# Kernel optimization log

Measured on AMD Instinct MI355X. Metric: run time of the kernel, lower is better.

Reference implementation:

```python
import jax, jax.numpy as jnp
import numpy as np

N = 10000   # nodes
E = 160000  # edges
IN_DIM, HID, OUT_DIM = 512, 512, 256


def setup_inputs() -> dict:
    key = jax.random.key(0)
    ks = jax.random.split(key, 10)
    x = jax.random.normal(ks[0], (N, IN_DIM), dtype=jnp.float32)
    edge_index = jax.random.randint(ks[1], (2, E), 0, N, dtype=jnp.int32)
    s = 0.05
    return {
        "x": x,
        "edge_index": edge_index,
        # GIN inner MLP (iVAE-style MLP with n_layers=1 == single Linear)
        "f_W": jax.random.normal(ks[2], (IN_DIM, HID), jnp.float32) * s,
        "f_b": jnp.zeros((HID,), jnp.float32),
        # GCNConv linear
        "gcn_W": jax.random.normal(ks[3], (IN_DIM + HID, OUT_DIM), jnp.float32) * s,
        "gcn_b": jnp.zeros((OUT_DIM,), jnp.float32),
        # decode MLP: out_dim -> out_dim/2 -> 2 with relu between
        "d1_W": jax.random.normal(ks[4], (OUT_DIM, OUT_DIM // 2), jnp.float32) * s,
        "d1_b": jnp.zeros((OUT_DIM // 2,), jnp.float32),
        "d2_W": jax.random.normal(ks[5], (OUT_DIM // 2, 2), jnp.float32) * s,
        "d2_b": jnp.zeros((2,), jnp.float32),
    }


def reference(x, edge_index, f_W, f_b, gcn_W, gcn_b, d1_W, d1_b, d2_W, d2_b):
    src, dst = edge_index[0], edge_index[1]

    # ---- GINConv(f, eps=-1.0): out = f((1+eps)*x + sum_{j in N(i)} x_j)
    # eps = -1 => (1+eps) = 0, so only the neighbor sum survives.
    agg = jax.ops.segment_sum(x[src], dst, num_segments=N)      # [N, in_dim]
    h1 = agg @ f_W + f_b                                        # [N, hid]

    # (the original computes z1 = (h1-mean)/std when regularize=True, but it is
    #  overwritten before being returned -> dead code, skipped)

    # ---- GCNConv on cat(x, h1) with self-loops + symmetric normalization
    xh = jnp.concatenate((x, h1), axis=1)                       # [N, in+hid]
    h = xh @ gcn_W                                              # [N, out]

    loop = jnp.arange(N, dtype=src.dtype)
    src_f = jnp.concatenate([src, loop])                        # [E+N]
    dst_f = jnp.concatenate([dst, loop])
    deg = jax.ops.segment_sum(jnp.ones_like(dst_f, jnp.float32), dst_f,
                              num_segments=N)                   # [N]
    dis = jnp.where(deg > 0, jax.lax.rsqrt(jnp.maximum(deg, 1.0)), 0.0)
    norm = dis[src_f] * dis[dst_f]                              # [E+N]
    out = jax.ops.segment_sum(h[src_f] * norm[:, None], dst_f,
                              num_segments=N) + gcn_b           # [N, out]

    # ---- decode MLP: Linear -> relu -> Linear
    z = jax.nn.relu(out @ d1_W + d1_b)
    z1 = z @ d2_W + d2_b                                        # [N, 2]
    return z1
```

## Files before the change

### kernel.cpp

```cpp
#include <hip/hip_runtime.h>

#define N_NODES 10000
#define E_EDGES 160000
#define IN_DIM  512
#define HID_DIM 512
#define OUT_DIM 256
#define MB_T    157

typedef __attribute__((ext_vector_type(8))) short short8;
typedef __attribute__((ext_vector_type(16))) float f32x16;
typedef unsigned short u16;

__device__ __forceinline__ u16 f2bh(float f) {
  union { float f; unsigned u; } v; v.f = f;
  return (u16)((v.u + 0x7FFFu + ((v.u >> 16) & 1u)) >> 16);
}
__device__ __forceinline__ float bh2f(u16 h) {
  union { unsigned u; float f; } v; v.u = ((unsigned)h) << 16;
  return v.f;
}

__device__ __forceinline__ size_t tidx(int mb, int ktTot, int kt, int c) {
  return ((size_t)(mb * ktTot + kt) * 256 + c) * 8;
}

#define GL_LDS(gsrc, ldst)                                                      \
  __builtin_amdgcn_global_load_lds(                                             \
      (const __attribute__((address_space(1))) unsigned int*)(gsrc),            \
      (__attribute__((address_space(3))) unsigned int*)(ldst), 16, 0, 0)

__global__ void count_kernel(const int* __restrict__ dst, int* __restrict__ cnt) {
  int e = blockIdx.x * 256 + threadIdx.x;
  if (e < E_EDGES) atomicAdd(&cnt[dst[e]], 1);
}

__global__ __launch_bounds__(1024) void scan_kernel(
    int* __restrict__ cnt, int* __restrict__ row, float* __restrict__ dis) {
  __shared__ int sums[1024];
  const int CH = 10;
  int t = threadIdx.x;
  int c[CH], excl[CH];
  int s = 0;
#pragma unroll
  for (int j = 0; j < CH; ++j) {
    int idx = t * CH + j;
    c[j] = (idx < N_NODES) ? cnt[idx] : 0;
    excl[j] = s;
    s += c[j];
  }
  sums[t] = s;
  __syncthreads();
  for (int off = 1; off < 1024; off <<= 1) {
    int v = (t >= off) ? sums[t - off] : 0;
    __syncthreads();
    if (t >= off) sums[t] += v;
    __syncthreads();
  }
  int base = (t == 0) ? 0 : sums[t - 1];
#pragma unroll
  for (int j = 0; j < CH; ++j) {
    int idx = t * CH + j;
    if (idx < N_NODES) {
      int start = base + excl[j];
      row[idx] = start;
      cnt[idx] = start;
      dis[idx] = rsqrtf((float)c[j] + 1.0f);
    }
  }
  if (t == 1023) row[N_NODES] = sums[1023];
}

__global__ void place_kernel(const int* __restrict__ src, const int* __restrict__ dst,
                             int* __restrict__ cursor, int* __restrict__ col) {
  int e = blockIdx.x * 256 + threadIdx.x;
  if (e < E_EDGES) {
    int pos = atomicAdd(&cursor[dst[e]], 1);
    col[pos] = src[e];
  }
}

#define PREP_PACKX  5000
#define PREP_PACKFW 5256
#define PREP_CONVT  5320
#define PREP_TOTAL  5336

__device__ __forceinline__ void pack_row(const float* __restrict__ src,
                                         u16* __restrict__ hi, u16* __restrict__ lo,
                                         int i, int tt) {
  int k0 = tt * 4;
  float4 v = *reinterpret_cast<const float4*>(src + (size_t)i * 512 + k0);
  float a[4] = {v.x, v.y, v.z, v.w};
  ushort4 h4, l4;
  u16* hp = &h4.x; u16* lp = &l4.x;
#pragma unroll
  for (int j = 0; j < 4; ++j) {
    u16 hh = f2bh(a[j]);
    hp[j] = hh;
    lp[j] = f2bh(a[j] - bh2f(hh));
  }
  int mb = i >> 6, rl = i & 63;
  int kt = k0 >> 5, si = (k0 >> 4) & 1, kh = (k0 >> 3) & 1;
  int c = (rl >> 5) * 128 + si * 64 + kh * 32 + (rl & 31);
  size_t idx = tidx(mb, 16, kt, c) + (k0 & 7);
  *reinterpret_cast<ushort4*>(hi + idx) = h4;
  *reinterpret_cast<ushort4*>(lo + idx) = l4;
}

__global__ __launch_bounds__(256) void prep_kernel(
    const float* __restrict__ x, const float* __restrict__ f_W,
    const float* __restrict__ gcn_W, const float* __restrict__ f_b,
    u16* __restrict__ x_hi, u16* __restrict__ x_lo,
    u16* __restrict__ fWp_hi, u16* __restrict__ fWp_lo,
    u16* __restrict__ Wcomb_hi, u16* __restrict__ Wcomb_lo,
    u16* __restrict__ WbotT_hi, u16* __restrict__ WbotT_lo,
    float* __restrict__ c2) {
  __shared__ float tile[64][65];
  int b = blockIdx.x, t = threadIdx.x;

  if (b < PREP_PACKX) {
    int i = b * 2 + (t >> 7);
    pack_row(x, x_hi, x_lo, i, t & 127);
  } else if (b < PREP_PACKFW) {
    int i = (b - PREP_PACKX) * 2 + (t >> 7);
    pack_row(f_W, fWp_hi, fWp_lo, i, t & 127);
  } else if (b < PREP_CONVT) {
    int lb = b - PREP_PACKFW;
    int part = lb >> 5;
    int li = lb & 31;
    int k0g = (li >> 2) * 64;
    int n0 = (li & 3) * 64;
    const float* W = part ? (gcn_W + (size_t)IN_DIM * OUT_DIM) : gcn_W;
    u16* hi = part ? WbotT_hi : Wcomb_hi;
    u16* lo = part ? WbotT_lo : Wcomb_lo;
    int lk = t >> 4, ln = (t & 15) * 4;
#pragma unroll
    for (int p = 0; p < 4; ++p) {
      float4 v = *reinterpret_cast<const float4*>(W + (size_t)(k0g + p * 16 + lk) * 256 + n0 + ln);
      tile[p * 16 + lk][ln + 0] = v.x;
      tile[p * 16 + lk][ln + 1] = v.y;
      tile[p * 16 + lk][ln + 2] = v.z;
      tile[p * 16 + lk][ln + 3] = v.w;
    }
    __syncthreads();
    int on = t >> 2;
    int ok = (t & 3) * 16;
    int colg = n0 + on;
    int nb = colg >> 6, rl = colg & 63;
#pragma unroll
    for (int q = 0; q < 4; ++q) {
      int kg = k0g + ok + q * 4;
      ushort4 h4, l4;
      u16* hq = &h4.x; u16* lq = &l4.x;
#pragma unroll
      for (int j = 0; j < 4; ++j) {
        float v = tile[ok + q * 4 + j][on];
        u16 hh = f2bh(v);
        hq[j] = hh;
        lq[j] = f2bh(v - bh2f(hh));
      }
      int kt = kg >> 5, si = (kg >> 4) & 1, kh = (kg >> 3) & 1;
      int c = (rl >> 5) * 128 + si * 64 + kh * 32 + (rl & 31);
      size_t idx = tidx(nb, 16, kt, c) + (kg & 7);
      *reinterpret_cast<ushort4*>(hi + idx) = h4;
      *reinterpret_cast<ushort4*>(lo + idx) = l4;
    }
  } else {
    int cb = b - PREP_CONVT;
    float s = 0.f;
    int kb = cb * 32;
#pragma unroll 8
    for (int k = kb; k < kb + 32; ++k)
      s += f_b[k] * gcn_W[(size_t)(IN_DIM + k) * OUT_DIM + t];
    atomicAdd(&c2[t], s);
  }
}

template <bool BIAS, bool OUT_TILED>
__global__ __launch_bounds__(256) void mfma_gemm4(
    const u16* __restrict__ Ah0, const u16* __restrict__ Al0,
    const u16* __restrict__ Ah1, const u16* __restrict__ Al1, int kSplit,
    const u16* __restrict__ Bh, const u16* __restrict__ Bl,
    const float* __restrict__ bias, float* __restrict__ C,
    u16* __restrict__ Ch, u16* __restrict__ Cl, int M, int K, int N,
    int mbOff) {
  __shared__ short8 S[2][1024];

  int t = threadIdx.x, w = t >> 6, l = t & 63;
  int wr = w >> 1, wc = w & 1;
  int mb = blockIdx.y, nb = blockIdx.x;
  int brow = mb * 64, bcol = nb * 64;
  int cid = w * 64 + l;

  f32x16 acc0, acc1;
#pragma unroll
  for (int r = 0; r < 16; ++r) { acc0[r] = 0.f; acc1[r] = 0.f; }

  int nt = K / 32;
  int ktTotB = K >> 5;
  int ktTot0 = kSplit >> 5;
  int ktTot1 = (K - kSplit) >> 5;

#define STAGE(BUF, K0)                                                         \
  {                                                                            \
    const u16 *Ah, *Al; size_t abase;                                          \
    if ((K0) < kSplit) {                                                       \
      Ah = Ah0; Al = Al0; abase = tidx(mb, ktTot0, (K0) >> 5, cid);            \
    } else {                                                                   \
      Ah = Ah1; Al = Al1; abase = tidx(mb, ktTot1, ((K0) - kSplit) >> 5, cid); \
    }                                                                          \
    size_t bbase = tidx(nb, ktTotB, (K0) >> 5, cid);                           \
    short8* base = &S[BUF][0] + w * 64;                                        \
    GL_LDS(Ah + abase, base);                                                  \
    GL_LDS(Al + abase, base + 256);                                            \
    GL_LDS(Bh + bbase, base + 512);                                            \
    GL_LDS(Bl + bbase, base + 768);                                            \
  }

  STAGE(0, 0)
  for (int ti = 0; ti < nt; ++ti) {
    int b = ti & 1;
    __syncthreads();
    if (ti + 1 < nt) STAGE(b ^ 1, (ti + 1) * 32)
    {
      short8 ah = S[b][wr * 128 + l];
      short8 al = S[b][256 + wr * 128 + l];
      short8 bh = S[b][512 + wc * 128 + l];
      short8 bl = S[b][768 + wc * 128 + l];
      acc0 = __builtin_amdgcn_mfma_f32_32x32x16_bf16(ah, bh, acc0, 0, 0, 0);
      acc0 = __builtin_amdgcn_mfma_f32_32x32x16_bf16(al, bh, acc0, 0, 0, 0);
      acc0 = __builtin_amdgcn_mfma_f32_32x32x16_bf16(ah, bl, acc0, 0, 0, 0);
    }
    {
      short8 ah = S[b][wr * 128 + 64 + l];
      short8 al = S[b][256 + wr * 128 + 64 + l];
      short8 bh = S[b][512 + wc * 128 + 64 + l];
      short8 bl = S[b][768 + wc * 128 + 64 + l];
      acc1 = __builtin_amdgcn_mfma_f32_32x32x16_bf16(ah, bh, acc1, 0, 0, 0);
      acc1 = __builtin_amdgcn_mfma_f32_32x32x16_bf16(al, bh, acc1, 0, 0, 0);
      acc1 = __builtin_amdgcn_mfma_f32_32x32x16_bf16(ah, bl, acc1, 0, 0, 0);
    }
  }
#undef STAGE

  f32x16 acc = acc0 + acc1;

  int r0l = wr * 32 + 4 * (l >> 5);
  int c0l = wc * 32 + (l & 31);

  if (OUT_TILED) {
    __syncthreads();
    u16* Hhi = (u16*)&S[0][0];
    u16* Hlo = Hhi + 4096;
    float badd = BIAS ? bias[bcol + c0l] : 0.f;
#pragma unroll
    for (int r = 0; r < 16; ++r) {
      int rl = r0l + (r & 3) + 8 * (r >> 2);
      float v = acc[r] + badd;
      u16 hh = f2bh(v);
      Hhi[rl * 64 + c0l] = hh;
      Hlo[rl * 64 + c0l] = f2bh(v - bh2f(hh));
    }
    __syncthreads();
    int ktTot = N >> 5;
#pragma unroll
    for (int pl = 0; pl < 2; ++pl) {
      const u16* Hs = pl ? Hlo : Hhi;
      u16* dA = pl ? Cl : Ch;
#pragma unroll
      for (int j = 0; j < 2; ++j) {
        int ci = t + j * 256;
        int ktl = ci >> 8;
        int c = ci & 255;
        int r = ((c >> 7) & 1) * 32 + (c & 31);
        int kloc = ktl * 32 + ((c >> 6) & 1) * 16 + ((c >> 5) & 1) * 8;
        short8 v = *reinterpret_cast<const short8*>(Hs + r * 64 + kloc);
        size_t db = tidx(mb + mbOff, ktTot, (bcol >> 5) + ktl, c);
        *reinterpret_cast<short8*>(dA + db) = v;
      }
    }
  } else {
    int colg = bcol + c0l;
    float badd = BIAS ? bias[colg] : 0.f;
#pragma unroll
    for (int r = 0; r < 16; ++r) {
      int rowg = brow + r0l + (r & 3) + 8 * (r >> 2);
      if (rowg < M) C[(size_t)rowg * N + colg] = acc[r] + badd;
    }
  }
}

template <int NB>
__global__ __launch_bounds__(256) void zgemm_kernel(
    const u16* __restrict__ Ah, const u16* __restrict__ Al,
    const u16* __restrict__ Bh, const u16* __restrict__ Bl,
    float* __restrict__ z1, u16* __restrict__ z2b, int M, int K) {
  constexpr int BCH = NB * 256;
  __shared__ short8 S[2][512 + 2 * BCH];

  int bid = blockIdx.x;
  int X = bid & 7, sslot = bid >> 3;
  int mb = X + 8 * (sslot >> 2);
  int nbB = sslot & 3;
  if (mb >= MB_T) return;

  int t = threadIdx.x, w = t >> 6, l = t & 63;
  int wr = w >> 1, wc = w & 1;
  int cid = t;
  int ktTot = K >> 5;

  f32x16 acc[NB][2];
#pragma unroll
  for (int n = 0; n < NB; ++n)
#pragma unroll
    for (int si = 0; si < 2; ++si)
#pragma unroll
      for (int r = 0; r < 16; ++r) acc[n][si][r] = 0.f;

  int nt = K / 32;

#define ZSTAGE(BUF, K0)                                                        \
  {                                                                            \
    size_t ab = tidx(mb, ktTot, (K0) >> 5, cid);                               \
    short8* base = &S[BUF][0] + w * 64;                                        \
    GL_LDS(Ah + ab, base);                                                     \
    GL_LDS(Al + ab, base + 256);                                               \
    _Pragma("unroll") for (int j = 0; j < NB; ++j) {                           \
      size_t bb = tidx(nbB * NB + j, ktTot, (K0) >> 5, cid);                   \
      GL_LDS(Bh + bb, base + 512 + j * 256);                                   \
      GL_LDS(Bl + bb, base + 512 + BCH + j * 256);                             \
    }                                                                          \
  }

  ZSTAGE(0, 0)
  for (int ti = 0; ti < nt; ++ti) {
    int b = ti & 1;
    __syncthreads();
    if (ti + 1 < nt) ZSTAGE(b ^ 1, (ti + 1) * 32)
#pragma unroll
    for (int si = 0; si < 2; ++si) {
      short8 ah = S[b][wr * 128 + si * 64 + l];
      short8 al = S[b][256 + wr * 128 + si * 64 + l];
#pragma unroll
      for (int n2 = 0; n2 < NB; ++n2) {
        short8 bh = S[b][512 + wc * 256 + n2 * 128 + si * 64 + l];
        short8 bl = S[b][512 + BCH + wc * 256 + n2 * 128 + si * 64 + l];
        acc[n2][si] = __builtin_amdgcn_mfma_f32_32x32x16_bf16(ah, bh, acc[n2][si], 0, 0, 0);
        acc[n2][si] = __builtin_amdgcn_mfma_f32_32x32x16_bf16(al, bh, acc[n2][si], 0, 0, 0);
        acc[n2][si] = __builtin_amdgcn_mfma_f32_32x32x16_bf16(ah, bl, acc[n2][si], 0, 0, 0);
      }
    }
  }
#undef ZSTAGE

  int r0 = mb * 64 + wr * 32 + 4 * (l >> 5);
#pragma unroll
  for (int n2 = 0; n2 < NB; ++n2) {
    f32x16 a = acc[n2][0] + acc[n2][1];
    int colg = nbB * (NB * 64) + wc * 64 + n2 * 32 + (l & 31);
#pragma unroll
    for (int r = 0; r < 16; ++r) {
      int rowg = r0 + (r & 3) + 8 * (r >> 2);
      if (rowg < M) {
        float v = a[r];
        if (colg < 256) z1[(size_t)rowg * 256 + colg] = v;
        else            z2b[(size_t)rowg * 256 + colg - 256] = f2bh(v);
      }
    }
  }
}

__global__ __launch_bounds__(64) void h_build_kernel(
    const float* __restrict__ z1, const u16* __restrict__ z2b,
    const int* __restrict__ row, const int* __restrict__ col,
    const float* __restrict__ c2, float* __restrict__ h,
    u16* __restrict__ h_bf) {
  int i = blockIdx.x, t = threadIdx.x;
  int half = t >> 5, sl = t & 31;
  int beg = row[i], end = row[i + 1];

  float a0[8] = {}, a1[8] = {}, a2[8] = {}, a3[8] = {};
  int e = beg + half;
  for (; e + 6 < end; e += 8) {
    int s0 = col[e], s1 = col[e + 2], s2 = col[e + 4], s3 = col[e + 6];
    short8 v0 = *reinterpret_cast<const short8*>(z2b + (size_t)s0 * 256 + sl * 8);
    short8 v1 = *reinterpret_cast<const short8*>(z2b + (size_t)s1 * 256 + sl * 8);
    short8 v2 = *reinterpret_cast<const short8*>(z2b + (size_t)s2 * 256 + sl * 8);
    short8 v3 = *reinterpret_cast<const short8*>(z2b + (size_t)s3 * 256 + sl * 8);
#pragma unroll
    for (int j = 0; j < 8; ++j) {
      a0[j] += bh2f((u16)v0[j]);
      a1[j] += bh2f((u16)v1[j]);
      a2[j] += bh2f((u16)v2[j]);
      a3[j] += bh2f((u16)v3[j]);
    }
  }
  for (; e < end; e += 2) {
    int s = col[e];
    short8 v = *reinterpret_cast<const short8*>(z2b + (size_t)s * 256 + sl * 8);
#pragma unroll
    for (int j = 0; j < 8; ++j) a0[j] += bh2f((u16)v[j]);
  }
  float acc[8];
#pragma unroll
  for (int j = 0; j < 8; ++j) {
    acc[j] = a0[j] + a1[j] + a2[j] + a3[j];
    acc[j] += __shfl_xor(acc[j], 32);
  }
  float4 z1a = *reinterpret_cast<const float4*>(z1 + (size_t)i * 256 + sl * 8);
  float4 z1b = *reinterpret_cast<const float4*>(z1 + (size_t)i * 256 + sl * 8 + 4);
  float4 ca = *reinterpret_cast<const float4*>(c2 + sl * 8);
  float4 cb = *reinterpret_cast<const float4*>(c2 + sl * 8 + 4);
  float hv[8] = {z1a.x + ca.x + acc[0], z1a.y + ca.y + acc[1],
                 z1a.z + ca.z + acc[2], z1a.w + ca.w + acc[3],
                 z1b.x + cb.x + acc[4], z1b.y + cb.y + acc[5],
                 z1b.z + cb.z + acc[6], z1b.w + cb.w + acc[7]};
  if (half == 0) {
    float4 o0{hv[0], hv[1], hv[2], hv[3]};
    float4 o1{hv[4], hv[5], hv[6], hv[7]};
    *reinterpret_cast<float4*>(h + (size_t)i * 256 + sl * 8) = o0;
    *reinterpret_cast<float4*>(h + (size_t)i * 256 + sl * 8 + 4) = o1;
    short8 hb;
#pragma unroll
    for (int j = 0; j < 8; ++j) hb[j] = (short)f2bh(hv[j]);
    *reinterpret_cast<short8*>(h_bf + (size_t)i * 256 + sl * 8) = hb;
  }
}

__global__ __launch_bounds__(64) void gcn_gather_kernel(
    const float* __restrict__ h, const u16* __restrict__ h_bf,
    const int* __restrict__ row, const int* __restrict__ col,
    const float* __restrict__ dis, const float* __restrict__ gcn_b,
    float* __restrict__ outg) {
  int i = blockIdx.x, t = threadIdx.x;
  int half = t >> 5, sl = t & 31;
  int beg = row[i], end = row[i + 1];
  float di = dis[i];

  float a0[8] = {}, a1[8] = {}, a2[8] = {}, a3[8] = {};
  int e = beg + half;
  for (; e + 6 < end; e += 8) {
    int s0 = col[e], s1 = col[e + 2], s2 = col[e + 4], s3 = col[e + 6];
    float w0 = dis[s0], w1 = dis[s1], w2 = dis[s2], w3 = dis[s3];
    short8 v0 = *reinterpret_cast<const short8*>(h_bf + (size_t)s0 * 256 + sl * 8);
    short8 v1 = *reinterpret_cast<const short8*>(h_bf + (size_t)s1 * 256 + sl * 8);
    short8 v2 = *reinterpret_cast<const short8*>(h_bf + (size_t)s2 * 256 + sl * 8);
    short8 v3 = *reinterpret_cast<const short8*>(h_bf + (size_t)s3 * 256 + sl * 8);
#pragma unroll
    for (int j = 0; j < 8; ++j) {
      a0[j] += w0 * bh2f((u16)v0[j]);
      a1[j] += w1 * bh2f((u16)v1[j]);
      a2[j] += w2 * bh2f((u16)v2[j]);
      a3[j] += w3 * bh2f((u16)v3[j]);
    }
  }
  for (; e < end; e += 2) {
    int s = col[e];
    float wv = dis[s];
    short8 v = *reinterpret_cast<const short8*>(h_bf + (size_t)s * 256 + sl * 8);
#pragma unroll
    for (int j = 0; j < 8; ++j) a0[j] += wv * bh2f((u16)v[j]);
  }
  float acc[8];
#pragma unroll
  for (int j = 0; j < 8; ++j) {
    acc[j] = a0[j] + a1[j] + a2[j] + a3[j];
    acc[j] += __shfl_xor(acc[j], 32);
  }
  if (half == 0) {
    float4 ha = *reinterpret_cast<const float4*>(h + (size_t)i * 256 + sl * 8);
    float4 hb = *reinterpret_cast<const float4*>(h + (size_t)i * 256 + sl * 8 + 4);
    float4 ba = *reinterpret_cast<const float4*>(gcn_b + sl * 8);
    float4 bb = *reinterpret_cast<const float4*>(gcn_b + sl * 8 + 4);
    float self = di * di;
    float4 o0{di * acc[0] + self * ha.x + ba.x, di * acc[1] + self * ha.y + ba.y,
              di * acc[2] + self * ha.z + ba.z, di * acc[3] + self * ha.w + ba.w};
    float4 o1{di * acc[4] + self * hb.x + bb.x, di * acc[5] + self * hb.y + bb.y,
              di * acc[6] + self * hb.z + bb.z, di * acc[7] + self * hb.w + bb.w};
    *reinterpret_cast<float4*>(outg + (size_t)i * 256 + sl * 8) = o0;
    *reinterpret_cast<float4*>(outg + (size_t)i * 256 + sl * 8 + 4) = o1;
  }
}

#define DEC_NODES 8
__global__ __launch_bounds__(128) void decode_kernel(
    const float* __restrict__ outg, const float* __restrict__ d1_W,
    const float* __restrict__ d1_b, const float* __restrict__ d2_W,
    const float* __restrict__ d2_b, float* __restrict__ z1) {
  __shared__ float rows[DEC_NODES][OUT_DIM];
  __shared__ float s0[128], s1[128];
  int t = threadIdx.x;
  int n0 = blockIdx.x * DEC_NODES;
#pragma unroll
  for (int j = 0; j < 4; ++j) {
    int idx = j * 512 + t * 4;
    *reinterpret_cast<float4*>(&rows[0][idx]) =
        *reinterpret_cast<const float4*>(outg + (size_t)n0 * OUT_DIM + idx);
  }
  __syncthreads();
  float acc[DEC_NODES];
  float b1 = d1_b[t];
#pragma unroll
  for (int n = 0; n < DEC_NODES; ++n) acc[n] = b1;
#pragma unroll 4
  for (int k = 0; k < OUT_DIM; ++k) {
    float wv = d1_W[k * 128 + t];
#pragma unroll
    for (int n = 0; n < DEC_NODES; ++n) acc[n] += rows[n][k] * wv;
  }
  float w0 = d2_W[t * 2 + 0], w1 = d2_W[t * 2 + 1];
  for (int n = 0; n < DEC_NODES; ++n) {
    float a = fmaxf(acc[n], 0.f);
    s0[t] = a * w0;
    s1[t] = a * w1;
    __syncthreads();
    for (int off = 64; off > 0; off >>= 1) {
      if (t < off) {
        s0[t] += s0[t + off];
        s1[t] += s1[t + off];
      }
      __syncthreads();
    }
    if (t == 0) {
      z1[(size_t)(n0 + n) * 2 + 0] = s0[0] + d2_b[0];
      z1[(size_t)(n0 + n) * 2 + 1] = s1[0] + d2_b[1];
    }
    __syncthreads();
  }
}

extern "C" void kernel_launch(void* const* d_in, const int* in_sizes, int n_in,
                              void* d_out, int out_size, void* d_ws, size_t ws_size,
                              hipStream_t stream) {
  const float* x     = (const float*)d_in[0];
  const int*   edge  = (const int*)d_in[1];
  const float* f_W   = (const float*)d_in[2];
  const float* f_b   = (const float*)d_in[3];
  const float* gcn_W = (const float*)d_in[4];
  const float* gcn_b = (const float*)d_in[5];
  const float* d1_W  = (const float*)d_in[6];
  const float* d1_b  = (const float*)d_in[7];
  const float* d2_W  = (const float*)d_in[8];
  const float* d2_b  = (const float*)d_in[9];
  float* out = (float*)d_out;
  char*  wsb = (char*)d_ws;

  const int* src = edge;
  const int* dst = edge + E_EDGES;

  const size_t TS   = (size_t)MB_T * 16 * 256 * 8 * sizeof(u16);
  const size_t WTLE = (size_t)16 * 256 * 8 * sizeof(u16);

  size_t o = 0;
  u16*   x_hi = (u16*)(wsb + o); o += TS;
  u16*   x_lo = (u16*)(wsb + o); o += TS;
  float* z1   = (float*)(wsb + o); o += (size_t)N_NODES * 256 * 4;
  u16*   z2b  = (u16*)(wsb + o);   o += (size_t)N_NODES * 256 * 2;
  float* h    = (float*)(wsb + o); o += (size_t)N_NODES * 256 * 4;
  u16*   h_bf = (u16*)(wsb + o);   o += (size_t)N_NODES * 256 * 2;
  float* dis7 = (float*)(wsb + o); o += (size_t)N_NODES * 4;
  int*   icnt7 = (int*)(wsb + o);  o += (size_t)N_NODES * 4;
  float* c2   = (float*)(wsb + o); o += OUT_DIM * 4;
  int*   irow7 = (int*)(wsb + o);  o += (size_t)(N_NODES + 1) * 4 + 12;
  int*   icol7 = (int*)(wsb + o);  o += (size_t)E_EDGES * 4;
  u16*   Wcomb_hi = (u16*)(wsb + o); o += 8 * WTLE;
  u16*   Wcomb_lo = (u16*)(wsb + o); o += 8 * WTLE;
  u16*   WbotT_hi = (u16*)(wsb + o); o += 4 * WTLE;
  u16*   WbotT_lo = (u16*)(wsb + o); o += 4 * WTLE;
  u16*   fWp_hi   = (u16*)(wsb + o); o += 8 * WTLE;
  u16*   fWp_lo   = (u16*)(wsb + o); o += 8 * WTLE;
  float* outg = (float*)(wsb + 0);
  const size_t v7_needed = o;

  if (ws_size >= v7_needed) {
    hipMemsetAsync(icnt7, 0, (size_t)N_NODES * sizeof(int) + OUT_DIM * sizeof(float), stream);
    count_kernel<<<(E_EDGES + 255) / 256, 256, 0, stream>>>(dst, icnt7);
    scan_kernel<<<1, 1024, 0, stream>>>(icnt7, irow7, dis7);
    place_kernel<<<(E_EDGES + 255) / 256, 256, 0, stream>>>(src, dst, icnt7, icol7);

    prep_kernel<<<PREP_TOTAL, 256, 0, stream>>>(
        x, f_W, gcn_W, f_b, x_hi, x_lo, fWp_hi, fWp_lo,
        Wcomb_hi, Wcomb_lo, WbotT_hi, WbotT_lo, c2);

    mfma_gemm4<false, true><<<dim3(512 / 64, 256 / 64), 256, 0, stream>>>(
        WbotT_hi, WbotT_lo, WbotT_hi, WbotT_lo, HID_DIM,
        fWp_hi, fWp_lo, nullptr, nullptr, Wcomb_hi, Wcomb_lo,
        256, HID_DIM, 512, 4);

    zgemm_kernel<2><<<640, 256, 0, stream>>>(
        x_hi, x_lo, Wcomb_hi, Wcomb_lo, z1, z2b, N_NODES, IN_DIM);

    h_build_kernel<<<N_NODES, 64, 0, stream>>>(z1, z2b, irow7, icol7, c2, h, h_bf);

    gcn_gather_kernel<<<N_NODES, 64, 0, stream>>>(h, h_bf, irow7, icol7, dis7, gcn_b, outg);
    decode_kernel<<<N_NODES / DEC_NODES, 128, 0, stream>>>(outg, d1_W, d1_b, d2_W, d2_b, out);
  }
}
```

Before: 150.2 us.

## Fuse graph-CSR build stages into prep and weight-GEMM kernels to cut launches

```diff
diff --git a/kernel.cpp b/kernel.cpp
--- a/kernel.cpp
+++ b/kernel.cpp
@@ -23,22 +23,21 @@
 __device__ __forceinline__ size_t tidx(int mb, int ktTot, int kt, int c) {
   return ((size_t)(mb * ktTot + kt) * 256 + c) * 8;
 }
+__device__ __forceinline__ short8 g16(const u16* p) {
+  return *reinterpret_cast<const short8*>(p);
+}
 
 #define GL_LDS(gsrc, ldst)                                                      \
   __builtin_amdgcn_global_load_lds(                                             \
       (const __attribute__((address_space(1))) unsigned int*)(gsrc),            \
       (__attribute__((address_space(3))) unsigned int*)(ldst), 16, 0, 0)
 
-__global__ void count_kernel(const int* __restrict__ dst, int* __restrict__ cnt) {
-  int e = blockIdx.x * 256 + threadIdx.x;
-  if (e < E_EDGES) atomicAdd(&cnt[dst[e]], 1);
-}
-
 __global__ __launch_bounds__(1024) void scan_kernel(
     int* __restrict__ cnt, int* __restrict__ row, float* __restrict__ dis) {
-  __shared__ int sums[1024];
+  __shared__ int wsum[16];
   const int CH = 10;
   int t = threadIdx.x;
+  int lane = t & 63, wid = t >> 6;
   int c[CH], excl[CH];
   int s = 0;
 #pragma unroll
@@ -48,15 +47,26 @@
     excl[j] = s;
     s += c[j];
   }
-  sums[t] = s;
+  int incl = s;
+#pragma unroll
+  for (int off = 1; off < 64; off <<= 1) {
+    int v = __shfl_up(incl, off);
+    if (lane >= off) incl += v;
+  }
+  if (lane == 63) wsum[wid] = incl;
   __syncthreads();
-  for (int off = 1; off < 1024; off <<= 1) {
-    int v = (t >= off) ? sums[t - off] : 0;
-    __syncthreads();
-    if (t >= off) sums[t] += v;
-    __syncthreads();
-  }
-  int base = (t == 0) ? 0 : sums[t - 1];
+  if (t < 16) {
+    int v = wsum[t];
+#pragma unroll
+    for (int off = 1; off < 16; off <<= 1) {
+      int u = __shfl_up(v, off);
+      if (t >= off) v += u;
+    }
+    wsum[t] = v;
+  }
+  __syncthreads();
+  int waveBase = (wid == 0) ? 0 : wsum[wid - 1];
+  int base = waveBase + incl - s;
 #pragma unroll
   for (int j = 0; j < CH; ++j) {
     int idx = t * CH + j;
@@ -67,22 +77,14 @@
       dis[idx] = rsqrtf((float)c[j] + 1.0f);
     }
   }
-  if (t == 1023) row[N_NODES] = sums[1023];
-}
-
-__global__ void place_kernel(const int* __restrict__ src, const int* __restrict__ dst,
-                             int* __restrict__ cursor, int* __restrict__ col) {
-  int e = blockIdx.x * 256 + threadIdx.x;
-  if (e < E_EDGES) {
-    int pos = atomicAdd(&cursor[dst[e]], 1);
-    col[pos] = src[e];
-  }
+  if (t == 1023) row[N_NODES] = wsum[15];
 }
 
 #define PREP_PACKX  5000
 #define PREP_PACKFW 5256
 #define PREP_CONVT  5320
-#define PREP_TOTAL  5336
+#define PREP_C2END  5336
+#define PREP_TOTAL  5961
 
 __device__ __forceinline__ void pack_row(const float* __restrict__ src,
                                          u16* __restrict__ hi, u16* __restrict__ lo,
@@ -109,6 +111,7 @@
 __global__ __launch_bounds__(256) void prep_kernel(
     const float* __restrict__ x, const float* __restrict__ f_W,
     const float* __restrict__ gcn_W, const float* __restrict__ f_b,
+    const int* __restrict__ dst, int* __restrict__ icnt,
     u16* __restrict__ x_hi, u16* __restrict__ x_lo,
     u16* __restrict__ fWp_hi, u16* __restrict__ fWp_lo,
     u16* __restrict__ Wcomb_hi, u16* __restrict__ Wcomb_lo,
@@ -164,7 +167,7 @@
       *reinterpret_cast<ushort4*>(hi + idx) = h4;
       *reinterpret_cast<ushort4*>(lo + idx) = l4;
     }
-  } else {
+  } else if (b < PREP_C2END) {
     int cb = b - PREP_CONVT;
     float s = 0.f;
     int kb = cb * 32;
@@ -172,119 +175,108 @@
     for (int k = kb; k < kb + 32; ++k)
       s += f_b[k] * gcn_W[(size_t)(IN_DIM + k) * OUT_DIM + t];
     atomicAdd(&c2[t], s);
-  }
-}
-
-template <bool BIAS, bool OUT_TILED>
-__global__ __launch_bounds__(256) void mfma_gemm4(
-    const u16* __restrict__ Ah0, const u16* __restrict__ Al0,
-    const u16* __restrict__ Ah1, const u16* __restrict__ Al1, int kSplit,
-    const u16* __restrict__ Bh, const u16* __restrict__ Bl,
-    const float* __restrict__ bias, float* __restrict__ C,
-    u16* __restrict__ Ch, u16* __restrict__ Cl, int M, int K, int N,
-    int mbOff) {
-  __shared__ short8 S[2][1024];
-
-  int t = threadIdx.x, w = t >> 6, l = t & 63;
+  } else {
+    int e = (b - PREP_C2END) * 256 + t;
+    if (e < E_EDGES) atomicAdd(&icnt[dst[e]], 1);
+  }
+}
+
+#define PW_PLACE 625
+#define PW_TOTAL 657
+
+__global__ __launch_bounds__(256) void pw_kernel(
+    const int* __restrict__ src, const int* __restrict__ dst,
+    int* __restrict__ cursor, int* __restrict__ col,
+    const u16* __restrict__ WbotT_hi, const u16* __restrict__ WbotT_lo,
+    const u16* __restrict__ fWp_hi, const u16* __restrict__ fWp_lo,
+    u16* __restrict__ Wcomb_hi, u16* __restrict__ Wcomb_lo) {
+  __shared__ u16 H[8192];
+  int b = blockIdx.x, t = threadIdx.x;
+
+  if (b < PW_PLACE) {
+    int e = b * 256 + t;
+    if (e < E_EDGES) {
+      int pos = atomicAdd(&cursor[dst[e]], 1);
+      col[pos] = src[e];
+    }
+    return;
+  }
+
+  int lb = b - PW_PLACE;
+  int nb = lb & 7;
+  int mbw = lb >> 3;
+  int w = t >> 6, l = t & 63;
   int wr = w >> 1, wc = w & 1;
-  int mb = blockIdx.y, nb = blockIdx.x;
-  int brow = mb * 64, bcol = nb * 64;
-  int cid = w * 64 + l;
+  int cA = wr * 128 + l;
+  int cB = wc * 128 + l;
 
   f32x16 acc0, acc1;
 #pragma unroll
   for (int r = 0; r < 16; ++r) { acc0[r] = 0.f; acc1[r] = 0.f; }
 
-  int nt = K / 32;
-  int ktTotB = K >> 5;
-  int ktTot0 = kSplit >> 5;
-  int ktTot1 = (K - kSplit) >> 5;
-
-#define STAGE(BUF, K0)                                                         \
+#define W2LOAD(KT, AH0, AL0, BH0, BL0, AH1, AL1, BH1, BL1)                     \
   {                                                                            \
-    const u16 *Ah, *Al; size_t abase;                                          \
-    if ((K0) < kSplit) {                                                       \
-      Ah = Ah0; Al = Al0; abase = tidx(mb, ktTot0, (K0) >> 5, cid);            \
-    } else {                                                                   \
-      Ah = Ah1; Al = Al1; abase = tidx(mb, ktTot1, ((K0) - kSplit) >> 5, cid); \
-    }                                                                          \
-    size_t bbase = tidx(nb, ktTotB, (K0) >> 5, cid);                           \
-    short8* base = &S[BUF][0] + w * 64;                                        \
-    GL_LDS(Ah + abase, base);                                                  \
-    GL_LDS(Al + abase, base + 256);                                            \
-    GL_LDS(Bh + bbase, base + 512);                                            \
-    GL_LDS(Bl + bbase, base + 768);                                            \
-  }
-
-  STAGE(0, 0)
-  for (int ti = 0; ti < nt; ++ti) {
-    int b = ti & 1;
-    __syncthreads();
-    if (ti + 1 < nt) STAGE(b ^ 1, (ti + 1) * 32)
-    {
-      short8 ah = S[b][wr * 128 + l];
-      short8 al = S[b][256 + wr * 128 + l];
-      short8 bh = S[b][512 + wc * 128 + l];
-      short8 bl = S[b][768 + wc * 128 + l];
-      acc0 = __builtin_amdgcn_mfma_f32_32x32x16_bf16(ah, bh, acc0, 0, 0, 0);
-      acc0 = __builtin_amdgcn_mfma_f32_32x32x16_bf16(al, bh, acc0, 0, 0, 0);
-      acc0 = __builtin_amdgcn_mfma_f32_32x32x16_bf16(ah, bl, acc0, 0, 0, 0);
-    }
-    {
-      short8 ah = S[b][wr * 128 + 64 + l];
-      short8 al = S[b][256 + wr * 128 + 64 + l];
-      short8 bh = S[b][512 + wc * 128 + 64 + l];
-      short8 bl = S[b][768 + wc * 128 + 64 + l];
-      acc1 = __builtin_amdgcn_mfma_f32_32x32x16_bf16(ah, bh, acc1, 0, 0, 0);
-      acc1 = __builtin_amdgcn_mfma_f32_32x32x16_bf16(al, bh, acc1, 0, 0, 0);
-      acc1 = __builtin_amdgcn_mfma_f32_32x32x16_bf16(ah, bl, acc1, 0, 0, 0);
-    }
-  }
-#undef STAGE
+    size_t a0 = tidx(mbw, 16, (KT), cA);                                       \
+    size_t a1 = tidx(mbw, 16, (KT), cA + 64);                                  \
+    size_t b0 = tidx(nb, 16, (KT), cB);                                        \
+    size_t b1 = tidx(nb, 16, (KT), cB + 64);                                   \
+    AH0 = g16(WbotT_hi + a0); AL0 = g16(WbotT_lo + a0);                        \
+    BH0 = g16(fWp_hi + b0);   BL0 = g16(fWp_lo + b0);                          \
+    AH1 = g16(WbotT_hi + a1); AL1 = g16(WbotT_lo + a1);                        \
+    BH1 = g16(fWp_hi + b1);   BL1 = g16(fWp_lo + b1);                          \
+  }
+#define W2MMA(AH0, AL0, BH0, BL0, AH1, AL1, BH1, BL1)                          \
+  {                                                                            \
+    acc0 = __builtin_amdgcn_mfma_f32_32x32x16_bf16(AH0, BH0, acc0, 0, 0, 0);   \
+    acc0 = __builtin_amdgcn_mfma_f32_32x32x16_bf16(AL0, BH0, acc0, 0, 0, 0);   \
+    acc0 = __builtin_amdgcn_mfma_f32_32x32x16_bf16(AH0, BL0, acc0, 0, 0, 0);   \
+    acc1 = __builtin_amdgcn_mfma_f32_32x32x16_bf16(AH1, BH1, acc1, 0, 0, 0);   \
+    acc1 = __builtin_amdgcn_mfma_f32_32x32x16_bf16(AL1, BH1, acc1, 0, 0, 0);   \
+    acc1 = __builtin_amdgcn_mfma_f32_32x32x16_bf16(AH1, BL1, acc1, 0, 0, 0);   \
+  }
+
+  short8 xah0, xal0, xbh0, xbl0, xah1, xal1, xbh1, xbl1;
+  short8 yah0, yal0, ybh0, ybl0, yah1, yal1, ybh1, ybl1;
+  W2LOAD(0, xah0, xal0, xbh0, xbl0, xah1, xal1, xbh1, xbl1)
+#pragma unroll
+  for (int kt = 0; kt < 16; kt += 2) {
+    W2LOAD(kt + 1, yah0, yal0, ybh0, ybl0, yah1, yal1, ybh1, ybl1)
+    W2MMA(xah0, xal0, xbh0, xbl0, xah1, xal1, xbh1, xbl1)
+    if (kt + 2 < 16)
+      W2LOAD(kt + 2, xah0, xal0, xbh0, xbl0, xah1, xal1, xbh1, xbl1)
+    W2MMA(yah0, yal0, ybh0, ybl0, yah1, yal1, ybh1, ybl1)
+  }
+#undef W2LOAD
+#undef W2MMA
 
   f32x16 acc = acc0 + acc1;
-
+  u16* Hhi = H;
+  u16* Hlo = H + 4096;
   int r0l = wr * 32 + 4 * (l >> 5);
   int c0l = wc * 32 + (l & 31);
-
-  if (OUT_TILED) {
-    __syncthreads();
-    u16* Hhi = (u16*)&S[0][0];
-    u16* Hlo = Hhi + 4096;
-    float badd = BIAS ? bias[bcol + c0l] : 0.f;
-#pragma unroll
-    for (int r = 0; r < 16; ++r) {
-      int rl = r0l + (r & 3) + 8 * (r >> 2);
-      float v = acc[r] + badd;
-      u16 hh = f2bh(v);
-      Hhi[rl * 64 + c0l] = hh;
-      Hlo[rl * 64 + c0l] = f2bh(v - bh2f(hh));
-    }
-    __syncthreads();
-    int ktTot = N >> 5;
-#pragma unroll
-    for (int pl = 0; pl < 2; ++pl) {
-      const u16* Hs = pl ? Hlo : Hhi;
-      u16* dA = pl ? Cl : Ch;
-#pragma unroll
-      for (int j = 0; j < 2; ++j) {
-        int ci = t + j * 256;
-        int ktl = ci >> 8;
-        int c = ci & 255;
-        int r = ((c >> 7) & 1) * 32 + (c & 31);
-        int kloc = ktl * 32 + ((c >> 6) & 1) * 16 + ((c >> 5) & 1) * 8;
-        short8 v = *reinterpret_cast<const short8*>(Hs + r * 64 + kloc);
-        size_t db = tidx(mb + mbOff, ktTot, (bcol >> 5) + ktl, c);
-        *reinterpret_cast<short8*>(dA + db) = v;
-      }
-    }
-  } else {
-    int colg = bcol + c0l;
-    float badd = BIAS ? bias[colg] : 0.f;
-#pragma unroll
-    for (int r = 0; r < 16; ++r) {
-      int rowg = brow + r0l + (r & 3) + 8 * (r >> 2);
-      if (rowg < M) C[(size_t)rowg * N + colg] = acc[r] + badd;
+#pragma unroll
+  for (int r = 0; r < 16; ++r) {
+    int rl = r0l + (r & 3) + 8 * (r >> 2);
+    float v = acc[r];
+    u16 hh = f2bh(v);
+    Hhi[rl * 64 + c0l] = hh;
+    Hlo[rl * 64 + c0l] = f2bh(v - bh2f(hh));
+  }
+  __syncthreads();
+#pragma unroll
+  for (int pl = 0; pl < 2; ++pl) {
+    const u16* Hs = pl ? Hlo : Hhi;
+    u16* dA = pl ? Wcomb_lo : Wcomb_hi;
+#pragma unroll
+    for (int j = 0; j < 2; ++j) {
+      int ci = t + j * 256;
+      int ktl = ci >> 8;
+      int c = ci & 255;
+      int r = ((c >> 7) & 1) * 32 + (c & 31);
+      int kloc = ktl * 32 + ((c >> 6) & 1) * 16 + ((c >> 5) & 1) * 8;
+      short8 v = *reinterpret_cast<const short8*>(Hs + r * 64 + kloc);
+      size_t db = tidx(mbw + 4, 16, nb * 2 + ktl, c);
+      *reinterpret_cast<short8*>(dA + db) = v;
     }
   }
 }
@@ -369,12 +361,13 @@
   }
 }
 
-__global__ __launch_bounds__(64) void h_build_kernel(
+__global__ __launch_bounds__(128) void h_build_kernel(
     const float* __restrict__ z1, const u16* __restrict__ z2b,
     const int* __restrict__ row, const int* __restrict__ col,
     const float* __restrict__ c2, float* __restrict__ h,
     u16* __restrict__ h_bf) {
-  int i = blockIdx.x, t = threadIdx.x;
+  int i = blockIdx.x * 2 + (threadIdx.x >> 6);
+  int t = threadIdx.x & 63;
   int half = t >> 5, sl = t & 31;
   int beg = row[i], end = row[i + 1];
 
@@ -426,12 +419,13 @@
   }
 }
 
-__global__ __launch_bounds__(64) void gcn_gather_kernel(
+__global__ __launch_bounds__(128) void gcn_gather_kernel(
     const float* __restrict__ h, const u16* __restrict__ h_bf,
     const int* __restrict__ row, const int* __restrict__ col,
     const float* __restrict__ dis, const float* __restrict__ gcn_b,
     float* __restrict__ outg) {
-  int i = blockIdx.x, t = threadIdx.x;
+  int i = blockIdx.x * 2 + (threadIdx.x >> 6);
+  int t = threadIdx.x & 63;
   int half = t >> 5, sl = t & 31;
   int beg = row[i], end = row[i + 1];
   float di = dis[i];
@@ -557,11 +551,11 @@
   u16*   z2b  = (u16*)(wsb + o);   o += (size_t)N_NODES * 256 * 2;
   float* h    = (float*)(wsb + o); o += (size_t)N_NODES * 256 * 4;
   u16*   h_bf = (u16*)(wsb + o);   o += (size_t)N_NODES * 256 * 2;
-  float* dis7 = (float*)(wsb + o); o += (size_t)N_NODES * 4;
-  int*   icnt7 = (int*)(wsb + o);  o += (size_t)N_NODES * 4;
+  float* dis8 = (float*)(wsb + o); o += (size_t)N_NODES * 4;
+  int*   icnt8 = (int*)(wsb + o);  o += (size_t)N_NODES * 4;
   float* c2   = (float*)(wsb + o); o += OUT_DIM * 4;
-  int*   irow7 = (int*)(wsb + o);  o += (size_t)(N_NODES + 1) * 4 + 12;
-  int*   icol7 = (int*)(wsb + o);  o += (size_t)E_EDGES * 4;
+  int*   irow8 = (int*)(wsb + o);  o += (size_t)(N_NODES + 1) * 4 + 12;
+  int*   icol8 = (int*)(wsb + o);  o += (size_t)E_EDGES * 4;
   u16*   Wcomb_hi = (u16*)(wsb + o); o += 8 * WTLE;
   u16*   Wcomb_lo = (u16*)(wsb + o); o += 8 * WTLE;
   u16*   WbotT_hi = (u16*)(wsb + o); o += 4 * WTLE;
@@ -569,29 +563,27 @@
   u16*   fWp_hi   = (u16*)(wsb + o); o += 8 * WTLE;
   u16*   fWp_lo   = (u16*)(wsb + o); o += 8 * WTLE;
   float* outg = (float*)(wsb + 0);
-  const size_t v7_needed = o;
-
-  if (ws_size >= v7_needed) {
-    hipMemsetAsync(icnt7, 0, (size_t)N_NODES * sizeof(int) + OUT_DIM * sizeof(float), stream);
-    count_kernel<<<(E_EDGES + 255) / 256, 256, 0, stream>>>(dst, icnt7);
-    scan_kernel<<<1, 1024, 0, stream>>>(icnt7, irow7, dis7);
-    place_kernel<<<(E_EDGES + 255) / 256, 256, 0, stream>>>(src, dst, icnt7, icol7);
+  const size_t v8_needed = o;
+
+  if (ws_size >= v8_needed) {
+    hipMemsetAsync(icnt8, 0, (size_t)N_NODES * sizeof(int) + OUT_DIM * sizeof(float), stream);
 
     prep_kernel<<<PREP_TOTAL, 256, 0, stream>>>(
-        x, f_W, gcn_W, f_b, x_hi, x_lo, fWp_hi, fWp_lo,
+        x, f_W, gcn_W, f_b, dst, icnt8, x_hi, x_lo, fWp_hi, fWp_lo,
         Wcomb_hi, Wcomb_lo, WbotT_hi, WbotT_lo, c2);
 
-    mfma_gemm4<false, true><<<dim3(512 / 64, 256 / 64), 256, 0, stream>>>(
-        WbotT_hi, WbotT_lo, WbotT_hi, WbotT_lo, HID_DIM,
-        fWp_hi, fWp_lo, nullptr, nullptr, Wcomb_hi, Wcomb_lo,
-        256, HID_DIM, 512, 4);
+    scan_kernel<<<1, 1024, 0, stream>>>(icnt8, irow8, dis8);
+
+    pw_kernel<<<PW_TOTAL, 256, 0, stream>>>(
+        src, dst, icnt8, icol8, WbotT_hi, WbotT_lo, fWp_hi, fWp_lo,
+        Wcomb_hi, Wcomb_lo);
 
     zgemm_kernel<2><<<640, 256, 0, stream>>>(
         x_hi, x_lo, Wcomb_hi, Wcomb_lo, z1, z2b, N_NODES, IN_DIM);
 
-    h_build_kernel<<<N_NODES, 64, 0, stream>>>(z1, z2b, irow7, icol7, c2, h, h_bf);
-
-    gcn_gather_kernel<<<N_NODES, 64, 0, stream>>>(h, h_bf, irow7, icol7, dis7, gcn_b, outg);
+    h_build_kernel<<<N_NODES / 2, 128, 0, stream>>>(z1, z2b, irow8, icol8, c2, h, h_bf);
+
+    gcn_gather_kernel<<<N_NODES / 2, 128, 0, stream>>>(h, h_bf, irow8, icol8, dis8, gcn_b, outg);
     decode_kernel<<<N_NODES / DEC_NODES, 128, 0, stream>>>(outg, d1_W, d1_b, d2_W, d2_b, out);
   }
 }
```

Result: faster. 142.5 us (-5.1%).
